# Kernel optimization log

Hardware: AMD Instinct MI355X
Metric: run time of the kernel (lower is better)

The kernel has to match this reference:

```python
import jax, jax.numpy as jnp
import numpy as np
import math

TOP_K = 2
CAPACITY_FACTOR = 1.25


def setup_inputs() -> dict:
    key = jax.random.key(0)
    ks = jax.random.split(key, 5)
    T, H, F, E = 16384, 1024, 4096, 8
    s = lambda d: 1.0 / np.sqrt(d)
    return {
        "tokens": jax.random.normal(ks[0], (T, H), jnp.float32),
        "w_router": jax.random.normal(ks[1], (H, E), jnp.float32) * s(H),
        "w_gate": jax.random.normal(ks[2], (E, H, F), jnp.float32) * s(H),
        "w_up": jax.random.normal(ks[3], (E, H, F), jnp.float32) * s(H),
        "w_down": jax.random.normal(ks[4], (E, F, H), jnp.float32) * s(F),
    }


def _moe_forward(tokens, w_router, w_gate, w_up, w_down):
    T, H = tokens.shape
    E = w_gate.shape[0]
    C = int(math.ceil(CAPACITY_FACTOR * T / E))  # per-expert capacity, static

    # --- Router: softmax over experts, top-k, renormalized weights ---
    logits = tokens @ w_router                       # (T, E)
    probs = jax.nn.softmax(logits, axis=-1)
    topv, topi = jax.lax.top_k(probs, TOP_K)         # (T, K)
    weights = topv / jnp.sum(topv, axis=-1, keepdims=True)

    # --- Dispatch ranks replicating torch loop order: k-slot major, token index minor ---
    onehot = jax.nn.one_hot(topi, E, dtype=jnp.int32)            # (T, K, E)
    counts = onehot.sum(axis=0)                                  # (K, E) tokens per (slot, expert)
    slot_off = jnp.concatenate(
        [jnp.zeros((1, E), jnp.int32), jnp.cumsum(counts, axis=0)[:-1]], axis=0
    )                                                            # (K, E) exclusive offset over k
    rank = jnp.cumsum(onehot, axis=0) - 1 + slot_off[None]       # (T, K, E)
    rank_tk = jnp.take_along_axis(rank, topi[..., None], axis=-1).squeeze(-1)  # (T, K)

    keep = rank_tk < C                                           # tokens beyond capacity are dropped
    slot = jnp.where(keep, rank_tk, C)                           # dropped -> trash slot C

    e_flat = topi.reshape(-1)                                    # (T*K,)
    s_flat = slot.reshape(-1)
    tok_rep = jnp.broadcast_to(tokens[:, None, :], (T, TOP_K, H)).reshape(-1, H)

    # Gather tokens into per-expert capacity buffers (extra trash row at slot C)
    buf = jnp.zeros((E, C + 1, H), tokens.dtype).at[e_flat, s_flat].set(tok_rep)
    x = buf[:, :C]                                               # (E, C, H)

    # --- SwiGLU expert FFN, batched over experts (grouped GEMM) ---
    h = jax.nn.silu(jnp.einsum('ech,ehf->ecf', x, w_gate)) * jnp.einsum('ech,ehf->ecf', x, w_up)
    y = jnp.einsum('ecf,efh->ech', h, w_down)                    # (E, C, H)

    # --- Weighted scatter back to token positions ---
    out_flat = y[e_flat, jnp.minimum(s_flat, C - 1)]             # (T*K, H)
    w_eff = (weights * keep.astype(weights.dtype)).reshape(-1, 1)
    return (out_flat * w_eff).reshape(T, TOP_K, H).sum(axis=1)   # (T, H)


def reference(tokens, w_router, w_gate, w_up, w_down):
    return _moe_forward(tokens, w_router, w_gate, w_up, w_down)
```

## Files before the change

### kernel.cpp

```cpp
#include <hip/hip_runtime.h>
#include <hip/hip_bf16.h>
#include <stdint.h>

#define T_TOK 16384
#define HDIM  1024
#define FDIM  4096
#define NE    8
#define CAP   2560

typedef __attribute__((ext_vector_type(8))) __bf16 bf16x8;
typedef __attribute__((ext_vector_type(4))) float  f32x4;

#define MFMA_BF16 __builtin_amdgcn_mfma_f32_16x16x32_bf16
#define VMCNT(n)  asm volatile("s_waitcnt vmcnt(" #n ")" ::: "memory")
#define LGKM0()   asm volatile("s_waitcnt lgkmcnt(0)" ::: "memory")
#define BAR()     __builtin_amdgcn_s_barrier()
#define SCHED0()  __builtin_amdgcn_sched_barrier(0)

__device__ __forceinline__ unsigned short f2bf(float f) {
  union { float f; unsigned u; } c; c.f = f;
  unsigned u = c.u;
  return (unsigned short)((u + 0x7FFFu + ((u >> 16) & 1u)) >> 16);
}

__device__ __forceinline__ void gload_lds16(const void* g, void* lds) {
  __builtin_amdgcn_global_load_lds((const __attribute__((address_space(1))) void*)g,
                                   (__attribute__((address_space(3))) void*)lds,
                                   16, 0, 0);
}

__global__ __launch_bounds__(256)
void transpose_cvt(const float* __restrict__ in, unsigned short* __restrict__ out,
                   int R, int Cc) {
  __shared__ unsigned short tile[64][68];
  int e  = blockIdx.z;
  int rb = blockIdx.y << 6, cb = blockIdx.x << 6;
  const float* inp = in + (size_t)e * R * Cc;
  unsigned short* op = out + (size_t)e * R * Cc;
  int lc  = threadIdx.x & 63;
  int lr0 = threadIdx.x >> 6;
#pragma unroll
  for (int rr = 0; rr < 64; rr += 4) {
    int r = rr + lr0;
    float v = inp[(size_t)(rb + r) * Cc + cb + lc];
    tile[lc][r] = f2bf(v);
  }
  __syncthreads();
  int c0 = threadIdx.x >> 3;
  int h0 = (threadIdx.x & 7) << 3;
#pragma unroll
  for (int cc = 0; cc < 64; cc += 32) {
    int c = cc + c0;
    uint2 v0 = *(const uint2*)&tile[c][h0];
    uint2 v1 = *(const uint2*)&tile[c][h0 + 4];
    uint4 v; v.x = v0.x; v.y = v0.y; v.z = v1.x; v.w = v1.y;
    *(uint4*)(op + (size_t)(cb + c) * R + rb + h0) = v;
  }
}

__global__ __launch_bounds__(256)
void transpose_cvt_gu(const float* __restrict__ in, unsigned short* __restrict__ out, int up) {
  __shared__ unsigned short tile[64][68];
  int e  = blockIdx.z;
  int rb = blockIdx.y << 6, cb = blockIdx.x << 6;
  const float* inp = in + (size_t)e * HDIM * FDIM;
  unsigned short* op = out + (size_t)e * 2 * FDIM * HDIM;
  int lc  = threadIdx.x & 63;
  int lr0 = threadIdx.x >> 6;
#pragma unroll
  for (int rr = 0; rr < 64; rr += 4) {
    int r = rr + lr0;
    float v = inp[(size_t)(rb + r) * FDIM + cb + lc];
    tile[lc][r] = f2bf(v);
  }
  __syncthreads();
  int c0 = threadIdx.x >> 3;
  int h0 = (threadIdx.x & 7) << 3;
#pragma unroll
  for (int cc = 0; cc < 64; cc += 32) {
    int c = cc + c0;
    int C = cb + c;
    int orow = ((C >> 5) << 6) + (C & 31) + (up << 5);
    uint2 v0 = *(const uint2*)&tile[c][h0];
    uint2 v1 = *(const uint2*)&tile[c][h0 + 4];
    uint4 v; v.x = v0.x; v.y = v0.y; v.z = v1.x; v.w = v1.y;
    *(uint4*)(op + (size_t)orow * HDIM + rb + h0) = v;
  }
}

__global__ __launch_bounds__(256)
void router_kernel(const float* __restrict__ tokens, const float* __restrict__ wr,
                   int* __restrict__ topsel, float* __restrict__ wts) {
  int lane = threadIdx.x & 63;
  int t = (blockIdx.x << 2) + (threadIdx.x >> 6);
  const float* tok = tokens + (size_t)t * HDIM;
  float acc[8];
#pragma unroll
  for (int i = 0; i < 8; ++i) acc[i] = 0.f;
#pragma unroll
  for (int j = 0; j < 4; ++j) {
    int h0 = j * 256 + lane * 4;
    float4 tv = *(const float4*)(tok + h0);
    const float* w = wr + (size_t)h0 * 8;
#pragma unroll
    for (int q = 0; q < 4; ++q) {
      float xv = ((const float*)&tv)[q];
      float4 wa = *(const float4*)(w + q * 8);
      float4 wb = *(const float4*)(w + q * 8 + 4);
      acc[0] += xv * wa.x; acc[1] += xv * wa.y; acc[2] += xv * wa.z; acc[3] += xv * wa.w;
      acc[4] += xv * wb.x; acc[5] += xv * wb.y; acc[6] += xv * wb.z; acc[7] += xv * wb.w;
    }
  }
#pragma unroll
  for (int off = 1; off < 64; off <<= 1) {
#pragma unroll
    for (int i = 0; i < 8; ++i) acc[i] += __shfl_xor(acc[i], off, 64);
  }
  if (lane == 0) {
    int e0 = 0; float v0 = acc[0];
#pragma unroll
    for (int i = 1; i < 8; ++i) if (acc[i] > v0) { v0 = acc[i]; e0 = i; }
    int e1 = -1; float v1 = -3.4e38f;
#pragma unroll
    for (int i = 0; i < 8; ++i) if (i != e0 && acc[i] > v1) { v1 = acc[i]; e1 = i; }
    float w0 = 1.f / (1.f + __expf(v1 - v0));
    topsel[t * 2] = e0; topsel[t * 2 + 1] = e1;
    wts[t * 2] = w0;    wts[t * 2 + 1] = 1.f - w0;
  }
}

__global__ __launch_bounds__(256)
void dispatch_kernel(const int* __restrict__ topsel, int* __restrict__ slot,
                     int* __restrict__ src_tok) {
  int e = blockIdx.x;
  int w = threadIdx.x >> 6, lane = threadIdx.x & 63;
  __shared__ int gcnt[2][256];
  __shared__ int tot[2];
#pragma unroll
  for (int k = 0; k < 2; ++k)
    for (int g = w; g < 256; g += 4) {
      int ch = topsel[(g * 64 + lane) * 2 + k];
      unsigned long long m = __ballot(ch == e);
      if (lane == 0) gcnt[k][g] = __popcll(m);
    }
  __syncthreads();
  if (w < 2) {
    int k = w;
    int c0 = gcnt[k][lane * 4], c1 = gcnt[k][lane * 4 + 1];
    int c2 = gcnt[k][lane * 4 + 2], c3 = gcnt[k][lane * 4 + 3];
    int s = c0 + c1 + c2 + c3;
    int inc = s;
#pragma unroll
    for (int off = 1; off < 64; off <<= 1) {
      int v = __shfl_up(inc, off, 64);
      if (lane >= off) inc += v;
    }
    int base = inc - s;
    gcnt[k][lane * 4] = base;
    gcnt[k][lane * 4 + 1] = base + c0;
    gcnt[k][lane * 4 + 2] = base + c0 + c1;
    gcnt[k][lane * 4 + 3] = base + c0 + c1 + c2;
    if (lane == 63) tot[k] = inc;
  }
  __syncthreads();
#pragma unroll
  for (int k = 0; k < 2; ++k) {
    int kbase = (k == 1) ? tot[0] : 0;
    for (int g = w; g < 256; g += 4) {
      int t = g * 64 + lane;
      int ch = topsel[t * 2 + k];
      unsigned long long m = __ballot(ch == e);
      if (ch == e) {
        unsigned long long lmask = lane ? (~0ull >> (64 - lane)) : 0ull;
        int r = kbase + gcnt[k][g] + __popcll(m & lmask);
        if (r < CAP) { slot[t * 2 + k] = r; src_tok[e * CAP + r] = t; }
        else         { slot[t * 2 + k] = -1; }
      }
    }
  }
}

__global__ __launch_bounds__(128)
void gather_x(const float* __restrict__ tokens, const int* __restrict__ src_tok,
              unsigned short* __restrict__ x) {
  int s = blockIdx.x;
  int t = src_tok[s];
  unsigned short* xr = x + (size_t)s * HDIM + threadIdx.x * 8;
  uint4 v = {0u, 0u, 0u, 0u};
  if (t >= 0) {
    const float* tr = tokens + (size_t)t * HDIM + threadIdx.x * 8;
    float4 a = *(const float4*)tr;
    float4 b = *(const float4*)(tr + 4);
    v.x = (unsigned)f2bf(a.x) | ((unsigned)f2bf(a.y) << 16);
    v.y = (unsigned)f2bf(a.z) | ((unsigned)f2bf(a.w) << 16);
    v.z = (unsigned)f2bf(b.x) | ((unsigned)f2bf(b.y) << 16);
    v.w = (unsigned)f2bf(b.z) | ((unsigned)f2bf(b.w) << 16);
  }
  *(uint4*)xr = v;
}

template<int BN>
__device__ __forceinline__ void mainloop8(const unsigned short* __restrict__ Ag,
                                          const unsigned short* __restrict__ Bg,
                                          int lda, int ldb, int nkt,
                                          unsigned short* lds, f32x4 (&acc)[4][BN / 32]) {
  constexpr int NF   = BN / 64;
  constexpr int AELB = 256 * 64 * 2;
  constexpr int BELB = BN * 64 * 2;
  constexpr int BHB  = (BN / 2) * 128;
  int tid = threadIdx.x, lane = tid & 63, wid = tid >> 6;
  int qr = wid >> 1, qc = wid & 1;
  int fr = lane & 15, fg = lane >> 4;

  char* ldsc = (char*)lds;
  int swz0 = ((fg       ^ (fr & 7)) << 4);
  int swz1 = (((4 | fg) ^ (fr & 7)) << 4);
  const char* a_b0 = ldsc + (qr * 32 + fr) * 128 + swz0;
  const char* a_b1 = ldsc + (qr * 32 + fr) * 128 + swz1;
  const char* b_b0 = ldsc + 2 * AELB + (qc * (NF * 16) + fr) * 128 + swz0;
  const char* b_b1 = ldsc + 2 * AELB + (qc * (NF * 16) + fr) * 128 + swz1;

  int srow = tid >> 3;
  int sl8  = ((tid & 7) ^ (srow & 7)) * 8;

  auto stA = [&](int mh, int kt, int pb) {
    char* dst = ldsc + pb + mh * 16384;
    gload_lds16(Ag + (size_t)(mh * 128 + srow) * lda + kt + sl8, dst + tid * 16);
    gload_lds16(Ag + (size_t)(mh * 128 + 64 + srow) * lda + kt + sl8, dst + tid * 16 + 8192);
  };
  auto stB = [&](int nh, int kt, int qb) {
    char* dst = ldsc + 2 * AELB + qb + nh * BHB;
    gload_lds16(Bg + (size_t)(nh * (BN / 2) + srow) * ldb + kt + sl8, dst + tid * 16);
    if constexpr (BN == 256)
      gload_lds16(Bg + (size_t)(nh * (BN / 2) + 64 + srow) * ldb + kt + sl8,
                  dst + tid * 16 + 8192);
  };

  bf16x8 aA[2][2], aB[2][2], bA[NF][2], bB[NF][2];
  auto rdA = [&](bf16x8 (&dst)[2][2], int mh, int pb) {
#pragma unroll
    for (int mf = 0; mf < 2; ++mf) {
      dst[mf][0] = *(const bf16x8*)(a_b0 + pb + mh * 16384 + mf * 2048);
      dst[mf][1] = *(const bf16x8*)(a_b1 + pb + mh * 16384 + mf * 2048);
    }
  };
  auto rdB = [&](bf16x8 (&dst)[NF][2], int nh, int qb) {
#pragma unroll
    for (int nf = 0; nf < NF; ++nf) {
      dst[nf][0] = *(const bf16x8*)(b_b0 + qb + nh * BHB + nf * 2048);
      dst[nf][1] = *(const bf16x8*)(b_b1 + qb + nh * BHB + nf * 2048);
    }
  };
  auto mmq = [&](bf16x8 (&A)[2][2], bf16x8 (&B)[NF][2], int mh, int nh) {
    __builtin_amdgcn_s_setprio(1);
#pragma unroll
    for (int mf = 0; mf < 2; ++mf)
#pragma unroll
      for (int nf = 0; nf < NF; ++nf)
#pragma unroll
        for (int kk = 0; kk < 2; ++kk)
          acc[mh * 2 + mf][nh * NF + nf] =
              MFMA_BF16(A[mf][kk], B[nf][kk], acc[mh * 2 + mf][nh * NF + nf], 0, 0, 0);
    __builtin_amdgcn_s_setprio(0);
  };

  int ktp = (nkt > 1 ? 64 : 0);
  stA(0, 0, 0); stB(0, 0, 0); stA(1, 0, 0); stB(1, 0, 0);
  stA(0, ktp, AELB); stB(1, ktp, BELB);
  if constexpr (BN == 256) VMCNT(4); else VMCNT(3);
  BAR();

  for (int t = 0; t < nkt; ++t) {
    int p0 = (t & 1) ? AELB : 0, p1 = AELB - p0;
    int q0 = (t & 1) ? BELB : 0, q1 = BELB - q0;
    int kt1 = ((t + 1 < nkt) ? t + 1 : nkt - 1) * 64;
    int kt2 = ((t + 2 < nkt) ? t + 2 : nkt - 1) * 64;

    rdA(aA, 0, p0); rdB(bA, 0, q0); rdA(aB, 1, p0);
    stB(0, kt1, q1);
    SCHED0();
    LGKM0();
    mmq(aA, bA, 0, 0);
    BAR();

    rdB(bB, 1, q0);
    stA(1, kt1, p1);
    SCHED0();
    mmq(aB, bA, 1, 0);
    LGKM0();
    BAR();

    stA(0, kt2, p0);
    mmq(aB, bB, 1, 1);
    BAR();

    stB(1, kt2, q0);
    mmq(aA, bB, 0, 1);
    if constexpr (BN == 256) VMCNT(4); else VMCNT(3);
    BAR();
  }
}

__global__ __launch_bounds__(512, 1)
void gemm1_kernel(const unsigned short* __restrict__ x, const unsigned short* __restrict__ wgu,
                  unsigned short* __restrict__ h) {
  __shared__ unsigned short lds[2 * 256 * 64 + 2 * 256 * 64];
  int flat = blockIdx.x;
  int e = flat & 7, idx = flat >> 3;
  int c = idx >> 4, i = idx & 15;
  int cbx = c / 5, cby = c % 5;
  int bx = cbx * 8 + (i & 7), by = cby * 2 + (i >> 3);
  const unsigned short* Ag = x   + ((size_t)e * CAP + (size_t)by * 256) * HDIM;
  const unsigned short* Bg = wgu + ((size_t)e * 2 * FDIM + (size_t)bx * 256) * HDIM;
  f32x4 acc[4][8];
#pragma unroll
  for (int m = 0; m < 4; ++m)
#pragma unroll
    for (int n = 0; n < 8; ++n) acc[m][n] = (f32x4){0.f, 0.f, 0.f, 0.f};
  mainloop8<256>(Ag, Bg, HDIM, HDIM, HDIM / 64, lds, acc);

  int lane = threadIdx.x & 63, wid = threadIdx.x >> 6;
  int qr = wid >> 1, qc = wid & 1, fr = lane & 15, fg = lane >> 4;
  size_t rbase = (size_t)e * CAP + by * 256;
#pragma unroll
  for (int mi = 0; mi < 4; ++mi) {
    int row0 = (mi >> 1) * 128 + qr * 32 + (mi & 1) * 16 + fg * 4;
#pragma unroll
    for (int nh = 0; nh < 2; ++nh)
#pragma unroll
      for (int nf = 0; nf < 2; ++nf) {
        int fcol = bx * 128 + (nh * 2 + qc) * 32 + nf * 16 + fr;
#pragma unroll
        for (int v = 0; v < 4; ++v) {
          float g = acc[mi][nh * 4 + nf][v];
          float u = acc[mi][nh * 4 + nf + 2][v];
          float s = g / (1.f + __expf(-g));
          h[(rbase + row0 + v) * FDIM + fcol] = f2bf(s * u);
        }
      }
  }
}

__global__ __launch_bounds__(512, 1)
void gemm2_kernel(const unsigned short* __restrict__ h, const unsigned short* __restrict__ wdT,
                  float* __restrict__ y) {
  __shared__ unsigned short lds[2 * 256 * 64 + 2 * 128 * 64];
  int flat = blockIdx.x;
  int e = flat & 7, idx = flat >> 3;
  int c = idx >> 4, i = idx & 15;
  int bx = i & 7, by = c * 2 + (i >> 3);
  const unsigned short* Ag = h   + ((size_t)e * CAP  + (size_t)by * 256) * FDIM;
  const unsigned short* Bg = wdT + ((size_t)e * HDIM + (size_t)bx * 128) * FDIM;
  f32x4 acc[4][4];
#pragma unroll
  for (int m = 0; m < 4; ++m)
#pragma unroll
    for (int n = 0; n < 4; ++n) acc[m][n] = (f32x4){0.f, 0.f, 0.f, 0.f};
  mainloop8<128>(Ag, Bg, FDIM, FDIM, FDIM / 64, lds, acc);

  int lane = threadIdx.x & 63, wid = threadIdx.x >> 6;
  int qr = wid >> 1, qc = wid & 1, fr = lane & 15, fg = lane >> 4;
  size_t rbase = (size_t)e * CAP + by * 256;
#pragma unroll
  for (int mi = 0; mi < 4; ++mi) {
    int row0 = (mi >> 1) * 128 + qr * 32 + (mi & 1) * 16 + fg * 4;
#pragma unroll
    for (int ni = 0; ni < 4; ++ni) {
      int col = bx * 128 + (ni >> 1) * 64 + qc * 32 + (ni & 1) * 16 + fr;
#pragma unroll
      for (int v = 0; v < 4; ++v)
        y[(rbase + row0 + v) * HDIM + col] = acc[mi][ni][v];
    }
  }
}

__global__ __launch_bounds__(256)
void combine_kernel(const float* __restrict__ y, const int* __restrict__ topsel,
                    const int* __restrict__ slot, const float* __restrict__ wts,
                    float* __restrict__ out) {
  int t = blockIdx.x;
  int i = threadIdx.x * 4;
  float4 s = {0.f, 0.f, 0.f, 0.f};
#pragma unroll
  for (int k = 0; k < 2; ++k) {
    int sl = slot[t * 2 + k];
    if (sl >= 0) {
      int e = topsel[t * 2 + k];
      float w = wts[t * 2 + k];
      float4 v = *(const float4*)(y + ((size_t)e * CAP + sl) * HDIM + i);
      s.x += w * v.x; s.y += w * v.y; s.z += w * v.z; s.w += w * v.w;
    }
  }
  *(float4*)(out + (size_t)t * HDIM + i) = s;
}

extern "C" void kernel_launch(void* const* d_in, const int* in_sizes, int n_in,
                              void* d_out, int out_size, void* d_ws, size_t ws_size,
                              hipStream_t stream) {
  const float* tokens   = (const float*)d_in[0];
  const float* w_router = (const float*)d_in[1];
  const float* w_gate   = (const float*)d_in[2];
  const float* w_up     = (const float*)d_in[3];
  const float* w_down   = (const float*)d_in[4];
  float* out = (float*)d_out;
  char* ws = (char*)d_ws;

  const size_t WGU = (size_t)NE * 2 * FDIM * HDIM * 2;
  const size_t WD  = (size_t)NE * HDIM * FDIM * 2;
  const size_t XB  = (size_t)NE * CAP * HDIM * 2;
  const size_t HB  = (size_t)NE * CAP * FDIM * 2;
  unsigned short* wguT = (unsigned short*)(ws);
  unsigned short* wdT  = (unsigned short*)(ws + WGU);
  unsigned short* xbuf = (unsigned short*)(ws + WGU + WD);
  unsigned short* hbuf = (unsigned short*)(ws + WGU + WD + XB);
  float* ybuf = (float*)(ws);
  char* tail = ws + WGU + WD + XB + HB;
  int*   topsel  = (int*)tail;
  float* wtsv    = (float*)(tail + (size_t)T_TOK * 2 * 4);
  int*   slotv   = (int*)(tail + (size_t)T_TOK * 2 * 8);
  int*   src_tok = (int*)(tail + (size_t)T_TOK * 2 * 12);

  hipMemsetAsync(src_tok, 0xFF, (size_t)NE * CAP * 4, stream);

  transpose_cvt_gu<<<dim3(FDIM / 64, HDIM / 64, NE), 256, 0, stream>>>(w_gate, wguT, 0);
  transpose_cvt_gu<<<dim3(FDIM / 64, HDIM / 64, NE), 256, 0, stream>>>(w_up,   wguT, 1);
  transpose_cvt<<<dim3(HDIM / 64, FDIM / 64, NE), 256, 0, stream>>>(w_down, wdT, FDIM, HDIM);

  router_kernel<<<T_TOK / 4, 256, 0, stream>>>(tokens, w_router, topsel, wtsv);
  dispatch_kernel<<<NE, 256, 0, stream>>>(topsel, slotv, src_tok);
  gather_x<<<NE * CAP, 128, 0, stream>>>(tokens, src_tok, xbuf);

  gemm1_kernel<<<2560, 512, 0, stream>>>(xbuf, wguT, hbuf);
  gemm2_kernel<<<640, 512, 0, stream>>>(hbuf, wdT, ybuf);

  combine_kernel<<<T_TOK, 256, 0, stream>>>(ybuf, topsel, slotv, wtsv, out);
}
```

Baseline: 807.6 us.

## Use split-K with 256x256 tiles in down-projection GEMM and bf16 partial outputs

The down-projection GEMM moves from 256x128 tiles over the full K=4096 to 256x256 tiles with a two-way split of K. Each half writes its partial result in bf16 to a separate buffer, and the combine kernel sums the two partials while applying the routing weights. The block count stays at 640, with larger tiles for better operand reuse, and output traffic is halved by using bf16 instead of fp32. In exchange, the result picks up extra bf16 rounding error, and combine now reads two buffers.

After: 746.8 us. 7.5% less time.

```diff
diff --git a/kernel.cpp b/kernel.cpp
--- a/kernel.cpp
+++ b/kernel.cpp
@@ -12,7 +12,8 @@
 typedef __attribute__((ext_vector_type(4))) float  f32x4;
 
 #define MFMA_BF16 __builtin_amdgcn_mfma_f32_16x16x32_bf16
-#define VMCNT(n)  asm volatile("s_waitcnt vmcnt(" #n ")" ::: "memory")
+#define VMCNT3()  asm volatile("s_waitcnt vmcnt(3)" ::: "memory")
+#define VMCNT4()  asm volatile("s_waitcnt vmcnt(4)" ::: "memory")
 #define LGKM0()   asm volatile("s_waitcnt lgkmcnt(0)" ::: "memory")
 #define BAR()     __builtin_amdgcn_s_barrier()
 #define SCHED0()  __builtin_amdgcn_sched_barrier(0)
@@ -21,6 +22,11 @@
   union { float f; unsigned u; } c; c.f = f;
   unsigned u = c.u;
   return (unsigned short)((u + 0x7FFFu + ((u >> 16) & 1u)) >> 16);
+}
+
+__device__ __forceinline__ float bf2f(unsigned short u) {
+  union { unsigned u; float f; } c; c.u = ((unsigned)u) << 16;
+  return c.f;
 }
 
 __device__ __forceinline__ void gload_lds16(const void* g, void* lds) {
@@ -267,7 +273,7 @@
   int ktp = (nkt > 1 ? 64 : 0);
   stA(0, 0, 0); stB(0, 0, 0); stA(1, 0, 0); stB(1, 0, 0);
   stA(0, ktp, AELB); stB(1, ktp, BELB);
-  if constexpr (BN == 256) VMCNT(4); else VMCNT(3);
+  if constexpr (BN == 256) VMCNT4(); else VMCNT3();
   BAR();
 
   for (int t = 0; t < nkt; ++t) {
@@ -296,7 +302,7 @@
 
     stB(1, kt2, q0);
     mmq(aA, bB, 0, 1);
-    if constexpr (BN == 256) VMCNT(4); else VMCNT(3);
+    if constexpr (BN == 256) VMCNT4(); else VMCNT3();
     BAR();
   }
 }
@@ -343,21 +349,23 @@
 
 __global__ __launch_bounds__(512, 1)
 void gemm2_kernel(const unsigned short* __restrict__ h, const unsigned short* __restrict__ wdT,
-                  float* __restrict__ y) {
-  __shared__ unsigned short lds[2 * 256 * 64 + 2 * 128 * 64];
+                  unsigned short* __restrict__ y0, unsigned short* __restrict__ y1) {
+  __shared__ unsigned short lds[2 * 256 * 64 + 2 * 256 * 64];
   int flat = blockIdx.x;
   int e = flat & 7, idx = flat >> 3;
-  int c = idx >> 4, i = idx & 15;
-  int bx = i & 7, by = c * 2 + (i >> 3);
-  const unsigned short* Ag = h   + ((size_t)e * CAP  + (size_t)by * 256) * FDIM;
-  const unsigned short* Bg = wdT + ((size_t)e * HDIM + (size_t)bx * 128) * FDIM;
-  f32x4 acc[4][4];
+  int ks = idx & 1, r2 = idx >> 1;
+  int bx = r2 & 3, by = r2 >> 2;
+  int k0 = ks * 2048;
+  const unsigned short* Ag = h   + ((size_t)e * CAP  + (size_t)by * 256) * FDIM + k0;
+  const unsigned short* Bg = wdT + ((size_t)e * HDIM + (size_t)bx * 256) * FDIM + k0;
+  f32x4 acc[4][8];
 #pragma unroll
   for (int m = 0; m < 4; ++m)
 #pragma unroll
-    for (int n = 0; n < 4; ++n) acc[m][n] = (f32x4){0.f, 0.f, 0.f, 0.f};
-  mainloop8<128>(Ag, Bg, FDIM, FDIM, FDIM / 64, lds, acc);
-
+    for (int n = 0; n < 8; ++n) acc[m][n] = (f32x4){0.f, 0.f, 0.f, 0.f};
+  mainloop8<256>(Ag, Bg, FDIM, FDIM, 2048 / 64, lds, acc);
+
+  unsigned short* yk = ks ? y1 : y0;
   int lane = threadIdx.x & 63, wid = threadIdx.x >> 6;
   int qr = wid >> 1, qc = wid & 1, fr = lane & 15, fg = lane >> 4;
   size_t rbase = (size_t)e * CAP + by * 256;
@@ -365,19 +373,21 @@
   for (int mi = 0; mi < 4; ++mi) {
     int row0 = (mi >> 1) * 128 + qr * 32 + (mi & 1) * 16 + fg * 4;
 #pragma unroll
-    for (int ni = 0; ni < 4; ++ni) {
-      int col = bx * 128 + (ni >> 1) * 64 + qc * 32 + (ni & 1) * 16 + fr;
-#pragma unroll
-      for (int v = 0; v < 4; ++v)
-        y[(rbase + row0 + v) * HDIM + col] = acc[mi][ni][v];
-    }
+    for (int nh = 0; nh < 2; ++nh)
+#pragma unroll
+      for (int nf = 0; nf < 4; ++nf) {
+        int col = bx * 256 + nh * 128 + qc * 64 + nf * 16 + fr;
+#pragma unroll
+        for (int v = 0; v < 4; ++v)
+          yk[(rbase + row0 + v) * HDIM + col] = f2bf(acc[mi][nh * 4 + nf][v]);
+      }
   }
 }
 
 __global__ __launch_bounds__(256)
-void combine_kernel(const float* __restrict__ y, const int* __restrict__ topsel,
-                    const int* __restrict__ slot, const float* __restrict__ wts,
-                    float* __restrict__ out) {
+void combine_kernel(const unsigned short* __restrict__ y0, const unsigned short* __restrict__ y1,
+                    const int* __restrict__ topsel, const int* __restrict__ slot,
+                    const float* __restrict__ wts, float* __restrict__ out) {
   int t = blockIdx.x;
   int i = threadIdx.x * 4;
   float4 s = {0.f, 0.f, 0.f, 0.f};
@@ -387,8 +397,13 @@
     if (sl >= 0) {
       int e = topsel[t * 2 + k];
       float w = wts[t * 2 + k];
-      float4 v = *(const float4*)(y + ((size_t)e * CAP + sl) * HDIM + i);
-      s.x += w * v.x; s.y += w * v.y; s.z += w * v.z; s.w += w * v.w;
+      size_t base = ((size_t)e * CAP + sl) * HDIM + i;
+      uint2 a = *(const uint2*)(y0 + base);
+      uint2 b = *(const uint2*)(y1 + base);
+      s.x += w * (bf2f((unsigned short)(a.x & 0xFFFF)) + bf2f((unsigned short)(b.x & 0xFFFF)));
+      s.y += w * (bf2f((unsigned short)(a.x >> 16))    + bf2f((unsigned short)(b.x >> 16)));
+      s.z += w * (bf2f((unsigned short)(a.y & 0xFFFF)) + bf2f((unsigned short)(b.y & 0xFFFF)));
+      s.w += w * (bf2f((unsigned short)(a.y >> 16))    + bf2f((unsigned short)(b.y >> 16)));
     }
   }
   *(float4*)(out + (size_t)t * HDIM + i) = s;
@@ -409,11 +424,13 @@
   const size_t WD  = (size_t)NE * HDIM * FDIM * 2;
   const size_t XB  = (size_t)NE * CAP * HDIM * 2;
   const size_t HB  = (size_t)NE * CAP * FDIM * 2;
+  const size_t YB  = (size_t)NE * CAP * HDIM * 2;
   unsigned short* wguT = (unsigned short*)(ws);
   unsigned short* wdT  = (unsigned short*)(ws + WGU);
   unsigned short* xbuf = (unsigned short*)(ws + WGU + WD);
   unsigned short* hbuf = (unsigned short*)(ws + WGU + WD + XB);
-  float* ybuf = (float*)(ws);
+  unsigned short* ybuf0 = (unsigned short*)(ws);
+  unsigned short* ybuf1 = (unsigned short*)(ws + YB);
   char* tail = ws + WGU + WD + XB + HB;
   int*   topsel  = (int*)tail;
   float* wtsv    = (float*)(tail + (size_t)T_TOK * 2 * 4);
@@ -431,7 +448,7 @@
   gather_x<<<NE * CAP, 128, 0, stream>>>(tokens, src_tok, xbuf);
 
   gemm1_kernel<<<2560, 512, 0, stream>>>(xbuf, wguT, hbuf);
-  gemm2_kernel<<<640, 512, 0, stream>>>(hbuf, wdT, ybuf);
-
-  combine_kernel<<<T_TOK, 256, 0, stream>>>(ybuf, topsel, slotv, wtsv, out);
-}
+  gemm2_kernel<<<640, 512, 0, stream>>>(hbuf, wdT, ybuf0, ybuf1);
+
+  combine_kernel<<<T_TOK, 256, 0, stream>>>(ybuf0, ybuf1, topsel, slotv, wtsv, out);
+}
```
